# Performance work log

Measured on AMD Instinct MI355X. Metric: run time of the kernel, lower is better.

Reference implementation:

```python
import jax, jax.numpy as jnp
import numpy as np

B, T, D_IN, EMB, H = 2, 2048, 1024, 1024, 16
HD = EMB // H  # head_dim = 64


def setup_inputs() -> dict:
    key = jax.random.key(0)
    ks = jax.random.split(key, 3)
    scale_qkv = 1.0 / np.sqrt(D_IN)
    scale_o = 1.0 / np.sqrt(EMB)
    return {
        "x": jax.random.normal(ks[0], (B, T, D_IN), dtype=jnp.float32),
        "W_qkv": jax.random.normal(ks[1], (D_IN, 3 * EMB), dtype=jnp.float32) * scale_qkv,
        "b_qkv": jnp.zeros((3 * EMB,), dtype=jnp.float32),
        "W_o": jax.random.normal(ks[2], (EMB, EMB), dtype=jnp.float32) * scale_o,
        "b_o": jnp.zeros((EMB,), dtype=jnp.float32),
    }


def reference(x, W_qkv, b_qkv, W_o, b_o):
    b, t, _ = x.shape
    qkv = x @ W_qkv + b_qkv                      # [B,T,3*EMB]
    # Match torch: reshape to (B,T,H,3*HD) -> permute -> chunk into q,k,v
    qkv = qkv.reshape(b, t, H, 3 * HD).transpose(0, 2, 1, 3)  # [B,H,T,3*HD]
    q, k, v = jnp.split(qkv, 3, axis=-1)         # each [B,H,T,HD]
    scale = 1.0 / jnp.sqrt(jnp.asarray(HD, dtype=q.dtype))
    scores = jnp.einsum("bhqd,bhkd->bhqk", q, k) * scale  # [B,H,T,T]
    attn = jax.nn.softmax(scores, axis=-1)
    values = jnp.einsum("bhqk,bhkd->bhqd", attn, v)       # [B,H,T,HD]
    values = values.transpose(0, 2, 1, 3).reshape(b, t, EMB)
    return values @ W_o + b_o
```

## Files before the change

### kernel.cpp

```cpp
#include <hip/hip_runtime.h>
#include <math.h>

typedef __bf16 bf16x8 __attribute__((ext_vector_type(8)));
typedef float f32x4 __attribute__((ext_vector_type(4)));

#define GPTR(p) ((const __attribute__((address_space(1))) void*)(p))
#define LPTR(p) ((__attribute__((address_space(3))) void*)(p))

#define QSCALE 0.18033688011112042f

__device__ __forceinline__ unsigned short f2bf(float f) {
  unsigned int u = __float_as_uint(f);
  u += 0x7FFFu + ((u >> 16) & 1u);
  return (unsigned short)(u >> 16);
}

__device__ __forceinline__ unsigned int pack_bf2(float lo, float hi) {
  return __builtin_amdgcn_perm(__float_as_uint(hi) + 0x8000u,
                               __float_as_uint(lo) + 0x8000u, 0x07060302u);
}

__device__ __forceinline__ float fast_exp2(float x) {
#if __has_builtin(__builtin_amdgcn_exp2f)
  return __builtin_amdgcn_exp2f(x);
#else
  return exp2f(x);
#endif
}

__device__ __forceinline__ f32x4 zero4() {
  f32x4 z; z[0] = 0.f; z[1] = 0.f; z[2] = 0.f; z[3] = 0.f; return z;
}

__global__ void conv_x_bf16(const float* __restrict__ in, unsigned short* __restrict__ out) {
  int i = (blockIdx.x * 256 + threadIdx.x) * 4;
  float4 v = *(const float4*)(in + i);
  ushort4 o;
  o.x = f2bf(v.x); o.y = f2bf(v.y); o.z = f2bf(v.z); o.w = f2bf(v.w);
  *(ushort4*)(out + i) = o;
}

__global__ void transpose_conv(const float* __restrict__ in, unsigned short* __restrict__ out,
                               int K, int N) {
  __shared__ float tile[64][65];
  int k0 = blockIdx.y * 64, n0 = blockIdx.x * 64;
  int t = threadIdx.x;
#pragma unroll
  for (int p = 0; p < 16; ++p) {
    int l = p * 256 + t; int r = l >> 6, c = l & 63;
    tile[r][c] = in[(size_t)(k0 + r) * N + n0 + c];
  }
  __syncthreads();
#pragma unroll
  for (int p = 0; p < 16; ++p) {
    int l = p * 256 + t; int r = l >> 6, c = l & 63;
    out[(size_t)(n0 + r) * K + k0 + c] = f2bf(tile[c][r]);
  }
}

__global__ __launch_bounds__(256) void gemm_qkv(
    const unsigned short* __restrict__ A, const unsigned short* __restrict__ Bt,
    const float* __restrict__ bias,
    unsigned short* __restrict__ Qd, unsigned short* __restrict__ Kd,
    unsigned short* __restrict__ Vtd) {
  __shared__ unsigned short As[128 * 32];
  __shared__ unsigned short Bs[128 * 32];
  const int tid = threadIdx.x, wave = tid >> 6, lane = tid & 63;
  const int quad = lane >> 4, l16 = lane & 15;
  const int wm = (wave >> 1) * 64, wn = (wave & 1) * 64;
  const int m0 = blockIdx.y * 128, n0 = blockIdx.x * 128;
  f32x4 acc[4][4];
#pragma unroll
  for (int i = 0; i < 4; ++i)
#pragma unroll
    for (int j = 0; j < 4; ++j) acc[i][j] = zero4();

  const int c = wave * 64 + lane;
  const int rA = c >> 2, o16 = (c & 3) * 8;

  for (int k0 = 0; k0 < 1024; k0 += 32) {
    __syncthreads();
    __builtin_amdgcn_global_load_lds(GPTR(A + (size_t)(m0 + rA) * 1024 + k0 + o16),
                                     LPTR(As + wave * 512), 16, 0, 0);
    __builtin_amdgcn_global_load_lds(GPTR(A + (size_t)(m0 + 64 + rA) * 1024 + k0 + o16),
                                     LPTR(As + 2048 + wave * 512), 16, 0, 0);
    __builtin_amdgcn_global_load_lds(GPTR(Bt + (size_t)(n0 + rA) * 1024 + k0 + o16),
                                     LPTR(Bs + wave * 512), 16, 0, 0);
    __builtin_amdgcn_global_load_lds(GPTR(Bt + (size_t)(n0 + 64 + rA) * 1024 + k0 + o16),
                                     LPTR(Bs + 2048 + wave * 512), 16, 0, 0);
    __syncthreads();
    bf16x8 af[4], bfr[4];
#pragma unroll
    for (int mt = 0; mt < 4; ++mt)
      af[mt] = *(const bf16x8*)(As + (wm + mt * 16 + l16) * 32 + quad * 8);
#pragma unroll
    for (int nt = 0; nt < 4; ++nt)
      bfr[nt] = *(const bf16x8*)(Bs + (wn + nt * 16 + l16) * 32 + quad * 8);
#pragma unroll
    for (int mt = 0; mt < 4; ++mt)
#pragma unroll
      for (int nt = 0; nt < 4; ++nt)
        acc[mt][nt] = __builtin_amdgcn_mfma_f32_16x16x32_bf16(af[mt], bfr[nt], acc[mt][nt], 0, 0, 0);
  }

#pragma unroll
  for (int mt = 0; mt < 4; ++mt) {
#pragma unroll
    for (int nt = 0; nt < 4; ++nt) {
      int m = m0 + wm + mt * 16 + quad * 4;
      int n = n0 + wn + nt * 16 + l16;
      float bv = bias[n];
      int h = n / 192, rem = n - h * 192;
      int which = rem >> 6, d = rem & 63;
      int b = m >> 11, t0 = m & 2047;
      size_t head = (size_t)(b * 16 + h);
      f32x4 a = acc[mt][nt];
      if (which == 0) {
        size_t base = (head * 2048 + t0) * 64 + d;
#pragma unroll
        for (int i = 0; i < 4; ++i)
          Qd[base + (size_t)i * 64] = f2bf((a[i] + bv) * QSCALE);
      } else if (which == 1) {
        size_t base = head * 131072 + (size_t)(t0 >> 6) * 4096;
#pragma unroll
        for (int i = 0; i < 4; ++i) {
          int tt = t0 + i;
          Kd[base + (tt & 63) * 64 + (((d >> 3) ^ (tt & 7)) << 3) + (d & 7)] = f2bf(a[i] + bv);
        }
      } else {
        size_t base = head * 131072 + (size_t)(t0 >> 6) * 4096;
        ushort4 o;
        o.x = f2bf(a[0] + bv); o.y = f2bf(a[1] + bv);
        o.z = f2bf(a[2] + bv); o.w = f2bf(a[3] + bv);
        *(ushort4*)(Vtd + base + d * 64 + (((((t0 & 63) >> 3)) ^ (d & 7)) << 3) + (t0 & 7)) = o;
      }
    }
  }
}

__global__ __launch_bounds__(256) void flash_attn(
    const unsigned short* __restrict__ Qg,
    const unsigned short* __restrict__ Kg,
    const unsigned short* __restrict__ Vg,
    unsigned short* __restrict__ att) {
  __shared__ unsigned short Ks[2][4096];
  __shared__ unsigned short Vs[2][4096];
  __shared__ unsigned short Ps[8192];
  const int tid = threadIdx.x, wave = tid >> 6, lane = tid & 63;
  const int quad = lane >> 4, l16 = lane & 15;
  const int h7 = l16 & 7;
  const int bh = blockIdx.y;
  const int q0 = blockIdx.x * 128 + wave * 32;

  bf16x8 bq[2][2];
#pragma unroll
  for (int qg = 0; qg < 2; ++qg)
#pragma unroll
    for (int kh = 0; kh < 2; ++kh)
      bq[qg][kh] = *(const bf16x8*)(Qg + ((size_t)bh * 2048 + q0 + qg * 16 + l16) * 64 + kh * 32 + quad * 8);

  f32x4 o[2][4];
#pragma unroll
  for (int qg = 0; qg < 2; ++qg)
#pragma unroll
    for (int i = 0; i < 4; ++i) o[qg][i] = zero4();
  float l_run[2] = {0.f, 0.f};

  unsigned short* pb = Ps + wave * 2048;
  const unsigned short* Kt = Kg + (size_t)bh * 131072 + lane * 8;
  const unsigned short* Vt = Vg + (size_t)bh * 131072 + lane * 8;
  const int so0 = wave * 512, so1 = (4 + wave) * 512;

#define STAGE_KV(buf, tile)                                                              \
  do {                                                                                   \
    const unsigned short* Kb_ = Kt + (tile) * 4096;                                      \
    const unsigned short* Vb_ = Vt + (tile) * 4096;                                      \
    __builtin_amdgcn_global_load_lds(GPTR(Kb_ + so0), LPTR(&Ks[buf][so0]), 16, 0, 0);    \
    __builtin_amdgcn_global_load_lds(GPTR(Kb_ + so1), LPTR(&Ks[buf][so1]), 16, 0, 0);    \
    __builtin_amdgcn_global_load_lds(GPTR(Vb_ + so0), LPTR(&Vs[buf][so0]), 16, 0, 0);    \
    __builtin_amdgcn_global_load_lds(GPTR(Vb_ + so1), LPTR(&Vs[buf][so1]), 16, 0, 0);    \
  } while (0)

  STAGE_KV(0, 0);
  __syncthreads();

  int cur = 0;
  for (int tile = 0; tile < 32; ++tile) {
    if (tile < 31) STAGE_KV(cur ^ 1, tile + 1);

    f32x4 s[2][4];
#pragma unroll
    for (int qg = 0; qg < 2; ++qg)
#pragma unroll
      for (int kt = 0; kt < 4; ++kt) s[qg][kt] = zero4();
#pragma unroll
    for (int kt = 0; kt < 4; ++kt) {
#pragma unroll
      for (int kh = 0; kh < 2; ++kh) {
        bf16x8 a = *(const bf16x8*)(&Ks[cur][(kt * 16 + l16) * 64 + (((kh * 4 + quad) ^ h7) << 3)]);
        s[0][kt] = __builtin_amdgcn_mfma_f32_16x16x32_bf16(a, bq[0][kh], s[0][kt], 0, 0, 0);
        s[1][kt] = __builtin_amdgcn_mfma_f32_16x16x32_bf16(a, bq[1][kh], s[1][kt], 0, 0, 0);
      }
    }

#pragma unroll
    for (int qg = 0; qg < 2; ++qg) {
      int qrow = qg * 16 + l16;
      float lsum = 0.f;
      float pv[4][4];
#pragma unroll
      for (int kt = 0; kt < 4; ++kt)
#pragma unroll
        for (int r = 0; r < 4; ++r) {
          float p = fast_exp2(s[qg][kt][r]);
          pv[kt][r] = p;
          lsum += p;
        }
#pragma unroll
      for (int kt = 0; kt < 4; ++kt) {
        uint2 pk;
        pk.x = pack_bf2(pv[kt][0], pv[kt][1]);
        pk.y = pack_bf2(pv[kt][2], pv[kt][3]);
        *(uint2*)(pb + qrow * 64 + (((2 * kt + (quad >> 1)) ^ h7) << 3) + (quad & 1) * 4) = pk;
      }
      lsum += __shfl_xor(lsum, 16);
      lsum += __shfl_xor(lsum, 32);
      l_run[qg] += lsum;
    }

#pragma unroll
    for (int st = 0; st < 2; ++st) {
      bf16x8 pf0 = *(const bf16x8*)(pb + (l16) * 64 + (((st * 4 + quad) ^ h7) << 3));
      bf16x8 pf1 = *(const bf16x8*)(pb + (16 + l16) * 64 + (((st * 4 + quad) ^ h7) << 3));
#pragma unroll
      for (int mt = 0; mt < 4; ++mt) {
        bf16x8 av = *(const bf16x8*)(&Vs[cur][(mt * 16 + l16) * 64 + (((st * 4 + quad) ^ h7) << 3)]);
        o[0][mt] = __builtin_amdgcn_mfma_f32_16x16x32_bf16(av, pf0, o[0][mt], 0, 0, 0);
        o[1][mt] = __builtin_amdgcn_mfma_f32_16x16x32_bf16(av, pf1, o[1][mt], 0, 0, 0);
      }
    }

    __syncthreads();
    cur ^= 1;
  }
#undef STAGE_KV

  int b = bh >> 4, h = bh & 15;
#pragma unroll
  for (int qg = 0; qg < 2; ++qg) {
    float inv_l = 1.f / l_run[qg];
    unsigned short* orow = att + ((size_t)b * 2048 + q0 + qg * 16 + l16) * 1024 + h * 64;
#pragma unroll
    for (int mt = 0; mt < 4; ++mt) {
      ushort4 ov;
      ov.x = f2bf(o[qg][mt][0] * inv_l);
      ov.y = f2bf(o[qg][mt][1] * inv_l);
      ov.z = f2bf(o[qg][mt][2] * inv_l);
      ov.w = f2bf(o[qg][mt][3] * inv_l);
      *(ushort4*)(orow + mt * 16 + quad * 4) = ov;
    }
  }
}

__global__ __launch_bounds__(256) void gemm_out(
    const unsigned short* __restrict__ A, const unsigned short* __restrict__ Bt,
    const float* __restrict__ bias, float* __restrict__ out) {
  __shared__ unsigned short As[128 * 32];
  __shared__ unsigned short Bs[64 * 32];
  const int tid = threadIdx.x, wave = tid >> 6, lane = tid & 63;
  const int quad = lane >> 4, l16 = lane & 15;
  const int wm = (wave >> 1) * 64, wn = (wave & 1) * 32;
  const int m0 = blockIdx.y * 128, n0 = blockIdx.x * 64;
  f32x4 acc[4][2];
#pragma unroll
  for (int i = 0; i < 4; ++i)
#pragma unroll
    for (int j = 0; j < 2; ++j) acc[i][j] = zero4();

  const int c = wave * 64 + lane;
  const int rA = c >> 2, o16 = (c & 3) * 8;

  for (int k0 = 0; k0 < 1024; k0 += 32) {
    __syncthreads();
    __builtin_amdgcn_global_load_lds(GPTR(A + (size_t)(m0 + rA) * 1024 + k0 + o16),
                                     LPTR(As + wave * 512), 16, 0, 0);
    __builtin_amdgcn_global_load_lds(GPTR(A + (size_t)(m0 + 64 + rA) * 1024 + k0 + o16),
                                     LPTR(As + 2048 + wave * 512), 16, 0, 0);
    __builtin_amdgcn_global_load_lds(GPTR(Bt + (size_t)(n0 + rA) * 1024 + k0 + o16),
                                     LPTR(Bs + wave * 512), 16, 0, 0);
    __syncthreads();
    bf16x8 af[4], bfr[2];
#pragma unroll
    for (int mt = 0; mt < 4; ++mt)
      af[mt] = *(const bf16x8*)(As + (wm + mt * 16 + l16) * 32 + quad * 8);
#pragma unroll
    for (int nt = 0; nt < 2; ++nt)
      bfr[nt] = *(const bf16x8*)(Bs + (wn + nt * 16 + l16) * 32 + quad * 8);
#pragma unroll
    for (int mt = 0; mt < 4; ++mt)
#pragma unroll
      for (int nt = 0; nt < 2; ++nt)
        acc[mt][nt] = __builtin_amdgcn_mfma_f32_16x16x32_bf16(af[mt], bfr[nt], acc[mt][nt], 0, 0, 0);
  }

#pragma unroll
  for (int mt = 0; mt < 4; ++mt) {
#pragma unroll
    for (int nt = 0; nt < 2; ++nt) {
      int m = m0 + wm + mt * 16 + quad * 4;
      int n = n0 + wn + nt * 16 + l16;
      float bv = bias[n];
      float* orow = out + (size_t)m * 1024 + n;
      orow[0]        = acc[mt][nt][0] + bv;
      orow[1024]     = acc[mt][nt][1] + bv;
      orow[2 * 1024] = acc[mt][nt][2] + bv;
      orow[3 * 1024] = acc[mt][nt][3] + bv;
    }
  }
}

extern "C" void kernel_launch(void* const* d_in, const int* in_sizes, int n_in,
                              void* d_out, int out_size, void* d_ws, size_t ws_size,
                              hipStream_t stream) {
  const float* x    = (const float*)d_in[0];
  const float* Wqkv = (const float*)d_in[1];
  const float* bqkv = (const float*)d_in[2];
  const float* Wo   = (const float*)d_in[3];
  const float* bo   = (const float*)d_in[4];
  float* out = (float*)d_out;

  unsigned short* xb    = (unsigned short*)d_ws;
  unsigned short* wqkvt = xb    + (size_t)4096 * 1024;
  unsigned short* wot   = wqkvt + (size_t)3072 * 1024;
  unsigned short* Qd    = wot   + (size_t)1024 * 1024;
  unsigned short* Kd    = Qd    + (size_t)32 * 2048 * 64;
  unsigned short* Vtd   = Kd    + (size_t)32 * 2048 * 64;
  unsigned short* attb  = Vtd   + (size_t)32 * 2048 * 64;

  conv_x_bf16<<<4096, 256, 0, stream>>>(x, xb);
  transpose_conv<<<dim3(48, 16), 256, 0, stream>>>(Wqkv, wqkvt, 1024, 3072);
  transpose_conv<<<dim3(16, 16), 256, 0, stream>>>(Wo, wot, 1024, 1024);
  gemm_qkv<<<dim3(24, 32), 256, 0, stream>>>(xb, wqkvt, bqkv, Qd, Kd, Vtd);
  flash_attn<<<dim3(16, 32), 256, 0, stream>>>(Qd, Kd, Vtd, attb);
  gemm_out<<<dim3(16, 32), 256, 0, stream>>>(attb, wot, bo, out);
}
```

Before: 214.5 us.

## Software-pipeline QK and softmax-PV across tiles; keep P in registers via permlane swaps

Restructures the flash-attention loop so the QK^T MFMAs for tile t+1 are issued alongside softmax and PV for tile t, using two score register sets and a triple-buffered V in LDS. The P matrix is no longer round-tripped through shared memory; it is rearranged into the MFMA operand layout with v_permlane32/16_swap instructions. This removes the LDS writes and reads for P and is meant to overlap exp work with matrix work. The cost is higher register pressure and more complex buffer indexing, with correctness depending on the permlane layout mapping.

New measurement: 212.9 us. About the same (-0.7%).

```diff
diff --git a/kernel.cpp b/kernel.cpp
--- a/kernel.cpp
+++ b/kernel.cpp
@@ -30,6 +30,13 @@
 
 __device__ __forceinline__ f32x4 zero4() {
   f32x4 z; z[0] = 0.f; z[1] = 0.f; z[2] = 0.f; z[3] = 0.f; return z;
+}
+
+__device__ __forceinline__ void permlane_swap32(unsigned int& a, unsigned int& b) {
+  asm("v_permlane32_swap_b32 %0, %1" : "+v"(a), "+v"(b));
+}
+__device__ __forceinline__ void permlane_swap16(unsigned int& a, unsigned int& b) {
+  asm("v_permlane16_swap_b32 %0, %1" : "+v"(a), "+v"(b));
 }
 
 __global__ void conv_x_bf16(const float* __restrict__ in, unsigned short* __restrict__ out) {
@@ -144,8 +151,7 @@
     const unsigned short* __restrict__ Vg,
     unsigned short* __restrict__ att) {
   __shared__ unsigned short Ks[2][4096];
-  __shared__ unsigned short Vs[2][4096];
-  __shared__ unsigned short Ps[8192];
+  __shared__ unsigned short Vs[3][4096];
   const int tid = threadIdx.x, wave = tid >> 6, lane = tid & 63;
   const int quad = lane >> 4, l16 = lane & 15;
   const int h7 = l16 & 7;
@@ -166,84 +172,123 @@
     for (int i = 0; i < 4; ++i) o[qg][i] = zero4();
   float l_run[2] = {0.f, 0.f};
 
-  unsigned short* pb = Ps + wave * 2048;
+  f32x4 sA[2][4], sB[2][4];
+
   const unsigned short* Kt = Kg + (size_t)bh * 131072 + lane * 8;
   const unsigned short* Vt = Vg + (size_t)bh * 131072 + lane * 8;
   const int so0 = wave * 512, so1 = (4 + wave) * 512;
 
-#define STAGE_KV(buf, tile)                                                              \
+#define STAGE_K(buf, tile)                                                               \
   do {                                                                                   \
     const unsigned short* Kb_ = Kt + (tile) * 4096;                                      \
-    const unsigned short* Vb_ = Vt + (tile) * 4096;                                      \
     __builtin_amdgcn_global_load_lds(GPTR(Kb_ + so0), LPTR(&Ks[buf][so0]), 16, 0, 0);    \
     __builtin_amdgcn_global_load_lds(GPTR(Kb_ + so1), LPTR(&Ks[buf][so1]), 16, 0, 0);    \
+  } while (0)
+#define STAGE_V(buf, tile)                                                               \
+  do {                                                                                   \
+    const unsigned short* Vb_ = Vt + (tile) * 4096;                                      \
     __builtin_amdgcn_global_load_lds(GPTR(Vb_ + so0), LPTR(&Vs[buf][so0]), 16, 0, 0);    \
     __builtin_amdgcn_global_load_lds(GPTR(Vb_ + so1), LPTR(&Vs[buf][so1]), 16, 0, 0);    \
   } while (0)
 
-  STAGE_KV(0, 0);
+#define QK(SN, KR)                                                                       \
+  do {                                                                                   \
+    _Pragma("unroll")                                                                    \
+    for (int qg = 0; qg < 2; ++qg)                                                       \
+      _Pragma("unroll")                                                                  \
+      for (int kt = 0; kt < 4; ++kt) SN[qg][kt] = zero4();                               \
+    _Pragma("unroll")                                                                    \
+    for (int kt = 0; kt < 4; ++kt) {                                                     \
+      _Pragma("unroll")                                                                  \
+      for (int kh = 0; kh < 2; ++kh) {                                                   \
+        bf16x8 a_ = *(const bf16x8*)(&Ks[KR][(kt * 16 + l16) * 64 + (((kh * 4 + quad) ^ h7) << 3)]); \
+        SN[0][kt] = __builtin_amdgcn_mfma_f32_16x16x32_bf16(a_, bq[0][kh], SN[0][kt], 0, 0, 0); \
+        SN[1][kt] = __builtin_amdgcn_mfma_f32_16x16x32_bf16(a_, bq[1][kh], SN[1][kt], 0, 0, 0); \
+      }                                                                                  \
+    }                                                                                    \
+  } while (0)
+
+#define SOFTMAX_PV(SP, VR)                                                               \
+  do {                                                                                   \
+    unsigned int pw_[2][4][2];                                                           \
+    _Pragma("unroll")                                                                    \
+    for (int qg = 0; qg < 2; ++qg) {                                                     \
+      float lsum_ = 0.f;                                                                 \
+      float pv_[4][4];                                                                   \
+      _Pragma("unroll")                                                                  \
+      for (int kt = 0; kt < 4; ++kt)                                                     \
+        _Pragma("unroll")                                                                \
+        for (int r = 0; r < 4; ++r) {                                                    \
+          float p_ = fast_exp2(SP[qg][kt][r]);                                           \
+          pv_[kt][r] = p_;                                                               \
+          lsum_ += p_;                                                                   \
+        }                                                                                \
+      _Pragma("unroll")                                                                  \
+      for (int kt = 0; kt < 4; ++kt) {                                                   \
+        pw_[qg][kt][0] = pack_bf2(pv_[kt][0], pv_[kt][1]);                               \
+        pw_[qg][kt][1] = pack_bf2(pv_[kt][2], pv_[kt][3]);                               \
+      }                                                                                  \
+      lsum_ += __shfl_xor(lsum_, 16);                                                    \
+      lsum_ += __shfl_xor(lsum_, 32);                                                    \
+      l_run[qg] += lsum_;                                                                \
+    }                                                                                    \
+    bf16x8 pf_[2][2];                                                                    \
+    _Pragma("unroll")                                                                    \
+    for (int qg = 0; qg < 2; ++qg) {                                                     \
+      _Pragma("unroll")                                                                  \
+      for (int st = 0; st < 2; ++st) {                                                   \
+        unsigned int a0_ = pw_[qg][2 * st][0], b0_ = pw_[qg][2 * st + 1][0];             \
+        unsigned int a1_ = pw_[qg][2 * st][1], b1_ = pw_[qg][2 * st + 1][1];             \
+        permlane_swap32(a0_, b0_); permlane_swap16(a0_, b0_);                            \
+        permlane_swap32(a1_, b1_); permlane_swap16(a1_, b1_);                            \
+        union { unsigned int u[4]; bf16x8 v; } x_;                                       \
+        x_.u[0] = a0_; x_.u[1] = a1_; x_.u[2] = b0_; x_.u[3] = b1_;                      \
+        pf_[qg][st] = x_.v;                                                              \
+      }                                                                                  \
+    }                                                                                    \
+    _Pragma("unroll")                                                                    \
+    for (int st = 0; st < 2; ++st) {                                                     \
+      _Pragma("unroll")                                                                  \
+      for (int mt = 0; mt < 4; ++mt) {                                                   \
+        bf16x8 av_ = *(const bf16x8*)(&Vs[VR][(mt * 16 + l16) * 64 + (((st * 4 + quad) ^ h7) << 3)]); \
+        o[0][mt] = __builtin_amdgcn_mfma_f32_16x16x32_bf16(av_, pf_[0][st], o[0][mt], 0, 0, 0); \
+        o[1][mt] = __builtin_amdgcn_mfma_f32_16x16x32_bf16(av_, pf_[1][st], o[1][mt], 0, 0, 0); \
+      }                                                                                  \
+    }                                                                                    \
+  } while (0)
+
+#define BODY(t, SP, SN, KR, KS)                                                          \
+  do {                                                                                   \
+    if ((t) < 31) { STAGE_K(KS, (t) + 1); STAGE_V(vn, (t) + 1); }                        \
+    int vr_ = vn + 1; if (vr_ == 3) vr_ = 0;                                             \
+    QK(SN, KR);                                                                          \
+    SOFTMAX_PV(SP, vr_);                                                                 \
+    __syncthreads();                                                                     \
+    vn = vr_;                                                                            \
+  } while (0)
+
+  STAGE_K(0, 0); STAGE_V(0, 0);
   __syncthreads();
-
-  int cur = 0;
-  for (int tile = 0; tile < 32; ++tile) {
-    if (tile < 31) STAGE_KV(cur ^ 1, tile + 1);
-
-    f32x4 s[2][4];
-#pragma unroll
-    for (int qg = 0; qg < 2; ++qg)
-#pragma unroll
-      for (int kt = 0; kt < 4; ++kt) s[qg][kt] = zero4();
-#pragma unroll
-    for (int kt = 0; kt < 4; ++kt) {
-#pragma unroll
-      for (int kh = 0; kh < 2; ++kh) {
-        bf16x8 a = *(const bf16x8*)(&Ks[cur][(kt * 16 + l16) * 64 + (((kh * 4 + quad) ^ h7) << 3)]);
-        s[0][kt] = __builtin_amdgcn_mfma_f32_16x16x32_bf16(a, bq[0][kh], s[0][kt], 0, 0, 0);
-        s[1][kt] = __builtin_amdgcn_mfma_f32_16x16x32_bf16(a, bq[1][kh], s[1][kt], 0, 0, 0);
-      }
-    }
-
-#pragma unroll
-    for (int qg = 0; qg < 2; ++qg) {
-      int qrow = qg * 16 + l16;
-      float lsum = 0.f;
-      float pv[4][4];
-#pragma unroll
-      for (int kt = 0; kt < 4; ++kt)
-#pragma unroll
-        for (int r = 0; r < 4; ++r) {
-          float p = fast_exp2(s[qg][kt][r]);
-          pv[kt][r] = p;
-          lsum += p;
-        }
-#pragma unroll
-      for (int kt = 0; kt < 4; ++kt) {
-        uint2 pk;
-        pk.x = pack_bf2(pv[kt][0], pv[kt][1]);
-        pk.y = pack_bf2(pv[kt][2], pv[kt][3]);
-        *(uint2*)(pb + qrow * 64 + (((2 * kt + (quad >> 1)) ^ h7) << 3) + (quad & 1) * 4) = pk;
-      }
-      lsum += __shfl_xor(lsum, 16);
-      lsum += __shfl_xor(lsum, 32);
-      l_run[qg] += lsum;
-    }
-
-#pragma unroll
-    for (int st = 0; st < 2; ++st) {
-      bf16x8 pf0 = *(const bf16x8*)(pb + (l16) * 64 + (((st * 4 + quad) ^ h7) << 3));
-      bf16x8 pf1 = *(const bf16x8*)(pb + (16 + l16) * 64 + (((st * 4 + quad) ^ h7) << 3));
-#pragma unroll
-      for (int mt = 0; mt < 4; ++mt) {
-        bf16x8 av = *(const bf16x8*)(&Vs[cur][(mt * 16 + l16) * 64 + (((st * 4 + quad) ^ h7) << 3)]);
-        o[0][mt] = __builtin_amdgcn_mfma_f32_16x16x32_bf16(av, pf0, o[0][mt], 0, 0, 0);
-        o[1][mt] = __builtin_amdgcn_mfma_f32_16x16x32_bf16(av, pf1, o[1][mt], 0, 0, 0);
-      }
-    }
-
-    __syncthreads();
-    cur ^= 1;
-  }
-#undef STAGE_KV
+  STAGE_K(1, 1); STAGE_V(1, 1);
+  QK(sA, 0);
+  __syncthreads();
+
+  int vn = 2;
+  for (int t = 1; t <= 29; t += 2) {
+    BODY(t, sA, sB, 1, 0);
+    BODY(t + 1, sB, sA, 0, 1);
+  }
+  BODY(31, sA, sB, 1, 0);
+
+  {
+    int vr_ = vn + 1; if (vr_ == 3) vr_ = 0;
+    SOFTMAX_PV(sB, vr_);
+  }
+#undef BODY
+#undef SOFTMAX_PV
+#undef QK
+#undef STAGE_K
+#undef STAGE_V
 
   int b = bh >> 4, h = bh & 15;
 #pragma unroll
```
